# Optimization experiments

Hardware: AMD Instinct MI355X
Metric: run time of the kernel (lower is better)

The kernel has to match this reference:

```python
import jax
import jax.numpy as jnp
from jax import lax
import numpy as np

E = 4          # num_experts
CIN = 128
COUT = 128
K = 3
STAT = 6
HID = 16       # router hidden width
STRIDE = 1
PAD = 1


def setup_inputs() -> dict:
    key = jax.random.key(0)
    ks = jax.random.split(key, 8)
    B, H, W = 32, 64, 64
    x = jax.random.normal(ks[0], (B, CIN, H, W), dtype=jnp.float32)
    scene_stats = jax.random.normal(ks[1], (B, STAT), dtype=jnp.float32)
    # router: Linear(stat_dim,16) -> ReLU -> Linear(16,E) -> Softmax
    W1 = jax.random.normal(ks[2], (HID, STAT), dtype=jnp.float32) * (1.0 / np.sqrt(STAT))
    b1 = jnp.zeros((HID,), dtype=jnp.float32)
    W2 = jax.random.normal(ks[3], (E, HID), dtype=jnp.float32) * (1.0 / np.sqrt(HID))
    b2 = jnp.zeros((E,), dtype=jnp.float32)
    weight_experts = jax.random.normal(ks[4], (E, COUT, CIN, K, K), dtype=jnp.float32) * 0.02
    bias_experts = jnp.zeros((E, COUT), dtype=jnp.float32)
    return {"x": x, "scene_stats": scene_stats, "W1": W1, "b1": b1,
            "W2": W2, "b2": b2, "weight_experts": weight_experts,
            "bias_experts": bias_experts}


def reference(x, scene_stats, W1, b1, W2, b2, weight_experts, bias_experts):
    B, Cin, H, W = x.shape
    Cout = weight_experts.shape[1]
    # router
    h = jax.nn.relu(scene_stats @ W1.T + b1)                 # [B, HID]
    routing = jax.nn.softmax(h @ W2.T + b2, axis=1)          # [B, E]
    # per-sample dynamic weights / bias
    dyn_w = jnp.einsum('bk,koihw->boihw', routing, weight_experts)  # [B,Cout,Cin,K,K]
    dyn_b = jnp.einsum('bk,ko->bo', routing, bias_experts)          # [B,Cout]
    # grouped conv with groups = B (each sample uses its own filter bank)
    x_r = x.reshape(1, B * Cin, H, W)
    w_r = dyn_w.reshape(B * Cout, Cin, K, K)
    out = lax.conv_general_dilated(
        x_r, w_r,
        window_strides=(STRIDE, STRIDE),
        padding=((PAD, PAD), (PAD, PAD)),
        feature_group_count=B,
        dimension_numbers=('NCHW', 'OIHW', 'NCHW'))
    out = out.reshape(B, Cout, out.shape[2], out.shape[3])
    return out + dyn_b[:, :, None, None]
```

## Files before the change

### kernel.cpp

```cpp
#include <hip/hip_runtime.h>
#include <hip/hip_bf16.h>


typedef short bf16x8 __attribute__((ext_vector_type(8)));
typedef float f32x4  __attribute__((ext_vector_type(4)));
typedef unsigned u32x4 __attribute__((ext_vector_type(4)));

#define VMWAIT(n) asm volatile("s_waitcnt vmcnt(" #n ")" ::: "memory")
#define LGKM0()   asm volatile("s_waitcnt lgkmcnt(0)" ::: "memory")

static __device__ __forceinline__ unsigned short f2bf(float f) {
    unsigned u = __float_as_uint(f);
    u = u + 0x7FFFu + ((u >> 16) & 1u);
    return (unsigned short)(u >> 16);
}

static __device__ __forceinline__ void gl2lds16(const unsigned short* g, unsigned short* l) {
    __builtin_amdgcn_global_load_lds(
        (const __attribute__((address_space(1))) unsigned int*)g,
        (__attribute__((address_space(3))) unsigned int*)l,
        16, 0, 0);
}

__global__ void prep_kernel(const float* __restrict__ stats, const float* __restrict__ W1,
                            const float* __restrict__ b1, const float* __restrict__ W2,
                            const float* __restrict__ b2, const float* __restrict__ wexp,
                            const float* __restrict__ bexp, unsigned short* __restrict__ dynw,
                            float* __restrict__ dynb)
{
    __shared__ float ls[4*1152];
    __shared__ float lr[32*4];
    const int tid = threadIdx.x;
    const int co  = blockIdx.x & 127;
    const int bg  = blockIdx.x >> 7;

    if (tid < 32) {
        float s[6];
#pragma unroll
        for (int i = 0; i < 6; ++i) s[i] = stats[tid*6 + i];
        float h[16];
#pragma unroll
        for (int j = 0; j < 16; ++j) {
            float a = b1[j];
#pragma unroll
            for (int i = 0; i < 6; ++i) a += W1[j*6+i]*s[i];
            h[j] = a > 0.f ? a : 0.f;
        }
        float lg[4];
#pragma unroll
        for (int e = 0; e < 4; ++e) {
            float a = b2[e];
#pragma unroll
            for (int j = 0; j < 16; ++j) a += W2[e*16+j]*h[j];
            lg[e] = a;
        }
        float m = fmaxf(fmaxf(lg[0],lg[1]), fmaxf(lg[2],lg[3]));
        float ex[4], sum = 0.f;
#pragma unroll
        for (int e = 0; e < 4; ++e) { ex[e] = expf(lg[e]-m); sum += ex[e]; }
        float inv = 1.f / sum;
#pragma unroll
        for (int e = 0; e < 4; ++e) lr[tid*4+e] = ex[e]*inv;
    }
    for (int i = tid; i < 4*1152; i += 256) {
        int e = i / 1152, j = i - e*1152;
        ls[i] = wexp[((unsigned long long)(e*128 + co))*1152 + j];
    }
    __syncthreads();

    if (bg == 0 && tid < 32) {
        float sb = 0.f;
#pragma unroll
        for (int e = 0; e < 4; ++e) sb += lr[tid*4+e] * bexp[e*128 + co];
        dynb[tid*128 + co] = sb;
    }

    const int ci  = tid & 127;
    const int tp0 = tid >> 7;
    const int cic = ci >> 5;
    const int g   = (ci >> 3) & 3;
    const int jj  = ci & 7;
    const int mi  = co >> 4;
    const int l15 = co & 15;
    for (int bb = bg*8; bb < bg*8 + 8; ++bb) {
        float r0 = lr[bb*4+0], r1 = lr[bb*4+1], r2 = lr[bb*4+2], r3 = lr[bb*4+3];
#pragma unroll
        for (int pp = 0; pp < 5; ++pp) {
            int tap = 2*pp + tp0;
            if (tap < 9) {
                int j = ci*9 + tap;
                float v = r0*ls[j] + r1*ls[1152+j] + r2*ls[2*1152+j] + r3*ls[3*1152+j];
                dynw[((((unsigned long long)(bb*4 + cic)*9 + tap)*8 + mi)*64 + g*16 + l15)*8 + jj] = f2bf(v);
            }
        }
    }
}

__global__ __launch_bounds__(256, 2) void conv_kernel(
    const float* __restrict__ x,
    const unsigned short* __restrict__ dynw,
    const float* __restrict__ dynb,
    float* __restrict__ out)
{
    __shared__ __align__(16) unsigned short xs[6*16*136];
    __shared__ __align__(16) unsigned short wsm[6][4096];

    const int tid  = threadIdx.x;
    const int wave = tid >> 6;
    const int lane = tid & 63;
    const int l15  = lane & 15;
    const int g    = lane >> 4;
    const int pr   = tid >> 4;
    const int c4   = tid & 15;

    int bidx = ((blockIdx.x & 7) << 6) | (blockIdx.x >> 3);
    const int b  = bidx >> 4;
    const int r0 = (bidx & 15) << 2;

    f32x4 acc[8][4];
#pragma unroll
    for (int mi = 0; mi < 8; ++mi)
#pragma unroll
        for (int ni = 0; ni < 4; ++ni) acc[mi][ni] = (f32x4){0.f,0.f,0.f,0.f};

    const float* xsrcb = x + (unsigned long long)b*(128ull*64*64);
    const unsigned short* wsrcb = dynw + (unsigned long long)b*(4ull*9*4096);

#define P1ISSUE(kk)                                                            \
    do {                                                                       \
        int grow_ = r0 + (kk) - 1;                                             \
        int growc_ = grow_ < 0 ? 0 : (grow_ > 63 ? 63 : grow_);                \
        const float* xp_ = xsrcb + (unsigned)((cic_*32 + 2*pr)*4096)           \
                         + growc_*64 + c4*4;                                   \
        xv[(kk)&1][0] = *(const float4*)xp_;                                   \
        xv[(kk)&1][1] = *(const float4*)(xp_ + 4096);                          \
    } while (0)

#define P1PROC(kk)                                                             \
    do {                                                                       \
        int grow_ = r0 + (kk) - 1;                                             \
        bool oob_ = (grow_ < 0) || (grow_ > 63);                               \
        float4 va_ = xv[(kk)&1][0], vb_ = xv[(kk)&1][1];                       \
        unsigned w0_ = oob_ ? 0u : (f2bf(va_.x) | ((unsigned)f2bf(vb_.x) << 16)); \
        unsigned w1_ = oob_ ? 0u : (f2bf(va_.y) | ((unsigned)f2bf(vb_.y) << 16)); \
        unsigned w2_ = oob_ ? 0u : (f2bf(va_.z) | ((unsigned)f2bf(vb_.z) << 16)); \
        unsigned w3_ = oob_ ? 0u : (f2bf(va_.w) | ((unsigned)f2bf(vb_.w) << 16)); \
        *(uint4*)((char*)xs + (kk)*4352 + pr*272 + c4*16)                      \
            = make_uint4(w0_, w1_, w2_, w3_);                                  \
    } while (0)

#define XSTAGE(CIC_, WFIRST_)                                                  \
    do {                                                                       \
        const int cic_ = (CIC_);                                               \
        _Pragma("unroll")                                                      \
        for (int t = 0; t < 3; ++t) {                                          \
            const unsigned short* wsrc_ = wsrcb + (unsigned)(((WFIRST_) + t)*4096); \
            unsigned short* wd_ = wsm[((WFIRST_) + t) % 6];                    \
            gl2lds16(wsrc_ + (unsigned)tid*8,       wd_ + (unsigned)tid*8);    \
            gl2lds16(wsrc_ + (unsigned)(tid+256)*8, wd_ + (unsigned)(tid+256)*8); \
        }                                                                      \
        {                                                                      \
            float4 xv[2][2];                                                   \
            P1ISSUE(0); P1ISSUE(1);                                            \
            VMWAIT(2); P1PROC(0); P1ISSUE(2);                                  \
            VMWAIT(2); P1PROC(1); P1ISSUE(3);                                  \
            VMWAIT(2); P1PROC(2); P1ISSUE(4);                                  \
            VMWAIT(2); P1PROC(3); P1ISSUE(5);                                  \
            VMWAIT(2); P1PROC(4);                                              \
            VMWAIT(0); P1PROC(5);                                              \
        }                                                                      \
        LGKM0();                                                               \
        __builtin_amdgcn_s_barrier();                                          \
        __builtin_amdgcn_sched_barrier(0);                                     \
    } while (0)

    if (tid < 96)
        *(uint4*)((char*)xs + (tid >> 4)*4352 + (tid & 15)*272 + 256)
            = make_uint4(0,0,0,0);
    XSTAGE(0, 0);

#pragma unroll
    for (int p = 0; p < 12; ++p) {
        const int cic = p / 3;
        if (p > 0) {
            VMWAIT(0);
            __builtin_amdgcn_s_barrier();
            __builtin_amdgcn_sched_barrier(0);
        }
        if ((p % 3) == 0 && p > 0) {
            XSTAGE(cic, 3*p + 3);
        } else if (p < 11) {
#pragma unroll
            for (int t = 0; t < 3; ++t) {
                const int s = 3*p + 3 + t;
                const unsigned short* wsrc = wsrcb + (unsigned)(s*4096);
                unsigned short* wd = wsm[s % 6];
                gl2lds16(wsrc + (unsigned)tid*8,       wd + (unsigned)tid*8);
                gl2lds16(wsrc + (unsigned)(tid+256)*8, wd + (unsigned)(tid+256)*8);
            }
        }
        const int ky   = p % 3;
        const int lrow = wave + ky;
        __builtin_amdgcn_s_setprio(1);
#pragma unroll
        for (int kx = 0; kx < 3; ++kx) {
            const unsigned short* wb = wsm[(3*p + kx) % 6];
            bf16x8 afrag[8];
#pragma unroll
            for (int mi = 0; mi < 8; ++mi)
                afrag[mi] = *(const bf16x8*)(wb + (unsigned)((mi*64 + lane)*8));
#pragma unroll
            for (int ni = 0; ni < 4; ++ni) {
                int c = 16*ni + l15 + kx - 1;
                int w = (c < 0) ? 65 : c;
                const char* bp = (const char*)xs + lrow*4352 + g*1088 + w*4;
                u32x4 bv;
                bv.x = *(const unsigned*)(bp);
                bv.y = *(const unsigned*)(bp + 272);
                bv.z = *(const unsigned*)(bp + 544);
                bv.w = *(const unsigned*)(bp + 816);
                bf16x8 bfrag = __builtin_bit_cast(bf16x8, bv);
#pragma unroll
                for (int mi = 0; mi < 8; ++mi)
                    acc[mi][ni] = __builtin_amdgcn_mfma_f32_16x16x32_bf16(
                                      afrag[mi], bfrag, acc[mi][ni], 0, 0, 0);
            }
        }
        __builtin_amdgcn_s_setprio(0);
    }

    const int y = r0 + wave;
#pragma unroll
    for (int mi = 0; mi < 8; ++mi) {
#pragma unroll
        for (int r = 0; r < 4; ++r) {
            int co = 16*mi + g*4 + r;
            float bias = dynb[b*128 + co];
            float* op = out + (((unsigned long long)(b*128 + co))*64 + y)*64;
#pragma unroll
            for (int ni = 0; ni < 4; ++ni)
                op[16*ni + l15] = acc[mi][ni][r] + bias;
        }
    }
#undef XSTAGE
#undef P1PROC
#undef P1ISSUE
}

extern "C" void kernel_launch(void* const* d_in, const int* in_sizes, int n_in,
                              void* d_out, int out_size, void* d_ws, size_t ws_size,
                              hipStream_t stream)
{
    const float* x     = (const float*)d_in[0];
    const float* stats = (const float*)d_in[1];
    const float* W1    = (const float*)d_in[2];
    const float* b1    = (const float*)d_in[3];
    const float* W2    = (const float*)d_in[4];
    const float* b2    = (const float*)d_in[5];
    const float* wexp  = (const float*)d_in[6];
    const float* bexp  = (const float*)d_in[7];
    float* out = (float*)d_out;

    char* ws = (char*)d_ws;
    float* dynb           = (float*)(ws + 512);
    unsigned short* dynw  = (unsigned short*)(ws + 32768);

    prep_kernel<<<512, 256, 0, stream>>>(stats, W1, b1, W2, b2, wexp, bexp, dynw, dynb);
    conv_kernel<<<512, 256, 0, stream>>>(x, dynw, dynb, out);
}
```

Before: 60.26 us.

## Prefetch next input-channel chunk into registers during MFMA phases

The fp32 input rows for the next input-channel chunk are now loaded into registers (6x2 float4) one phase early, overlapping their global latency with the MFMA work of the current phase. At the chunk boundary they are only converted to bf16 and written to LDS. Before, they were loaded and converted serially inside the stage. The MFMA inner loop is also reordered: all four B fragments are loaded first, then each A fragment is streamed once per mi. This raises register pressure from the 12 float4 buffers and could reduce occupancy or cause spills.

```diff
diff --git a/kernel.cpp b/kernel.cpp
--- a/kernel.cpp
+++ b/kernel.cpp
@@ -126,70 +126,63 @@
     const float* xsrcb = x + (unsigned long long)b*(128ull*64*64);
     const unsigned short* wsrcb = dynw + (unsigned long long)b*(4ull*9*4096);
 
-#define P1ISSUE(kk)                                                            \
+    float4 xv[6][2];
+
+#define P1ISSUE(CIC_, KK)                                                      \
     do {                                                                       \
-        int grow_ = r0 + (kk) - 1;                                             \
+        int grow_ = r0 + (KK) - 1;                                             \
         int growc_ = grow_ < 0 ? 0 : (grow_ > 63 ? 63 : grow_);                \
-        const float* xp_ = xsrcb + (unsigned)((cic_*32 + 2*pr)*4096)           \
+        const float* xp_ = xsrcb + (unsigned)(((CIC_)*32 + 2*pr)*4096)         \
                          + growc_*64 + c4*4;                                   \
-        xv[(kk)&1][0] = *(const float4*)xp_;                                   \
-        xv[(kk)&1][1] = *(const float4*)(xp_ + 4096);                          \
+        xv[KK][0] = *(const float4*)xp_;                                       \
+        xv[KK][1] = *(const float4*)(xp_ + 4096);                              \
     } while (0)
 
-#define P1PROC(kk)                                                             \
+#define P1PROC(KK)                                                             \
     do {                                                                       \
-        int grow_ = r0 + (kk) - 1;                                             \
+        int grow_ = r0 + (KK) - 1;                                             \
         bool oob_ = (grow_ < 0) || (grow_ > 63);                               \
-        float4 va_ = xv[(kk)&1][0], vb_ = xv[(kk)&1][1];                       \
+        float4 va_ = xv[KK][0], vb_ = xv[KK][1];                               \
         unsigned w0_ = oob_ ? 0u : (f2bf(va_.x) | ((unsigned)f2bf(vb_.x) << 16)); \
         unsigned w1_ = oob_ ? 0u : (f2bf(va_.y) | ((unsigned)f2bf(vb_.y) << 16)); \
         unsigned w2_ = oob_ ? 0u : (f2bf(va_.z) | ((unsigned)f2bf(vb_.z) << 16)); \
         unsigned w3_ = oob_ ? 0u : (f2bf(va_.w) | ((unsigned)f2bf(vb_.w) << 16)); \
-        *(uint4*)((char*)xs + (kk)*4352 + pr*272 + c4*16)                      \
+        *(uint4*)((char*)xs + (KK)*4352 + pr*272 + c4*16)                      \
             = make_uint4(w0_, w1_, w2_, w3_);                                  \
-    } while (0)
-
-#define XSTAGE(CIC_, WFIRST_)                                                  \
-    do {                                                                       \
-        const int cic_ = (CIC_);                                               \
-        _Pragma("unroll")                                                      \
-        for (int t = 0; t < 3; ++t) {                                          \
-            const unsigned short* wsrc_ = wsrcb + (unsigned)(((WFIRST_) + t)*4096); \
-            unsigned short* wd_ = wsm[((WFIRST_) + t) % 6];                    \
-            gl2lds16(wsrc_ + (unsigned)tid*8,       wd_ + (unsigned)tid*8);    \
-            gl2lds16(wsrc_ + (unsigned)(tid+256)*8, wd_ + (unsigned)(tid+256)*8); \
-        }                                                                      \
-        {                                                                      \
-            float4 xv[2][2];                                                   \
-            P1ISSUE(0); P1ISSUE(1);                                            \
-            VMWAIT(2); P1PROC(0); P1ISSUE(2);                                  \
-            VMWAIT(2); P1PROC(1); P1ISSUE(3);                                  \
-            VMWAIT(2); P1PROC(2); P1ISSUE(4);                                  \
-            VMWAIT(2); P1PROC(3); P1ISSUE(5);                                  \
-            VMWAIT(2); P1PROC(4);                                              \
-            VMWAIT(0); P1PROC(5);                                              \
-        }                                                                      \
-        LGKM0();                                                               \
-        __builtin_amdgcn_s_barrier();                                          \
-        __builtin_amdgcn_sched_barrier(0);                                     \
     } while (0)
 
     if (tid < 96)
         *(uint4*)((char*)xs + (tid >> 4)*4352 + (tid & 15)*272 + 256)
             = make_uint4(0,0,0,0);
-    XSTAGE(0, 0);
+    P1ISSUE(0,0); P1ISSUE(0,1); P1ISSUE(0,2);
+    P1ISSUE(0,3); P1ISSUE(0,4); P1ISSUE(0,5);
+#pragma unroll
+    for (int t = 0; t < 3; ++t) {
+        const unsigned short* wsrc = wsrcb + (unsigned)(t*4096);
+        gl2lds16(wsrc + (unsigned)tid*8,       wsm[t] + (unsigned)tid*8);
+        gl2lds16(wsrc + (unsigned)(tid+256)*8, wsm[t] + (unsigned)(tid+256)*8);
+    }
+    VMWAIT(6);
+    P1PROC(0); P1PROC(1); P1PROC(2); P1PROC(3); P1PROC(4); P1PROC(5);
+    VMWAIT(0);
+    LGKM0();
+    __builtin_amdgcn_s_barrier();
+    __builtin_amdgcn_sched_barrier(0);
 
 #pragma unroll
     for (int p = 0; p < 12; ++p) {
-        const int cic = p / 3;
         if (p > 0) {
             VMWAIT(0);
             __builtin_amdgcn_s_barrier();
             __builtin_amdgcn_sched_barrier(0);
         }
         if ((p % 3) == 0 && p > 0) {
-            XSTAGE(cic, 3*p + 3);
-        } else if (p < 11) {
+            P1PROC(0); P1PROC(1); P1PROC(2); P1PROC(3); P1PROC(4); P1PROC(5);
+            LGKM0();
+            __builtin_amdgcn_s_barrier();
+            __builtin_amdgcn_sched_barrier(0);
+        }
+        if (p < 11) {
 #pragma unroll
             for (int t = 0; t < 3; ++t) {
                 const int s = 3*p + 3 + t;
@@ -199,31 +192,37 @@
                 gl2lds16(wsrc + (unsigned)(tid+256)*8, wd + (unsigned)(tid+256)*8);
             }
         }
+        if ((p % 3) == 2 && p < 9) {
+            const int nc = p/3 + 1;
+            P1ISSUE(nc,0); P1ISSUE(nc,1); P1ISSUE(nc,2);
+            P1ISSUE(nc,3); P1ISSUE(nc,4); P1ISSUE(nc,5);
+            __builtin_amdgcn_sched_barrier(0);
+        }
         const int ky   = p % 3;
         const int lrow = wave + ky;
         __builtin_amdgcn_s_setprio(1);
 #pragma unroll
         for (int kx = 0; kx < 3; ++kx) {
             const unsigned short* wb = wsm[(3*p + kx) % 6];
-            bf16x8 afrag[8];
-#pragma unroll
-            for (int mi = 0; mi < 8; ++mi)
-                afrag[mi] = *(const bf16x8*)(wb + (unsigned)((mi*64 + lane)*8));
+            u32x4 bv[4];
 #pragma unroll
             for (int ni = 0; ni < 4; ++ni) {
                 int c = 16*ni + l15 + kx - 1;
                 int w = (c < 0) ? 65 : c;
                 const char* bp = (const char*)xs + lrow*4352 + g*1088 + w*4;
-                u32x4 bv;
-                bv.x = *(const unsigned*)(bp);
-                bv.y = *(const unsigned*)(bp + 272);
-                bv.z = *(const unsigned*)(bp + 544);
-                bv.w = *(const unsigned*)(bp + 816);
-                bf16x8 bfrag = __builtin_bit_cast(bf16x8, bv);
-#pragma unroll
-                for (int mi = 0; mi < 8; ++mi)
+                bv[ni].x = *(const unsigned*)(bp);
+                bv[ni].y = *(const unsigned*)(bp + 272);
+                bv[ni].z = *(const unsigned*)(bp + 544);
+                bv[ni].w = *(const unsigned*)(bp + 816);
+            }
+#pragma unroll
+            for (int mi = 0; mi < 8; ++mi) {
+                bf16x8 afrag = *(const bf16x8*)(wb + (unsigned)((mi*64 + lane)*8));
+#pragma unroll
+                for (int ni = 0; ni < 4; ++ni)
                     acc[mi][ni] = __builtin_amdgcn_mfma_f32_16x16x32_bf16(
-                                      afrag[mi], bfrag, acc[mi][ni], 0, 0, 0);
+                                      afrag, __builtin_bit_cast(bf16x8, bv[ni]),
+                                      acc[mi][ni], 0, 0, 0);
             }
         }
         __builtin_amdgcn_s_setprio(0);
@@ -242,7 +241,6 @@
                 op[16*ni + l15] = acc[mi][ni][r] + bias;
         }
     }
-#undef XSTAGE
 #undef P1PROC
 #undef P1ISSUE
 }
```

New measurement: 59.65 us. Within noise of the previous version (-1.0%).
